# Kernel optimization log

Hardware: AMD Instinct MI355X
Metric: run time of the kernel (lower is better)

The kernel has to match this reference:

```python
import jax, jax.numpy as jnp
import numpy as np

B, S, DIM = 2, 2048, 2048
H, HKV = 16, 4
HD = DIM // H          # 128
REP = H // HKV         # 4


def _rope_cos_sin(seq_len, head_dim, theta=10000.0):
    freqs = 1.0 / (theta ** (np.arange(0, head_dim, 2, dtype=np.float32) / head_dim))
    t = np.arange(seq_len, dtype=np.float32)
    ang = np.outer(t, freqs)  # (S, HD//2)
    return jnp.asarray(np.cos(ang)), jnp.asarray(np.sin(ang))


def setup_inputs() -> dict:
    key = jax.random.key(0)
    ks = jax.random.split(key, 5)
    cos, sin = _rope_cos_sin(S, HD)
    s = 1.0 / np.sqrt(DIM)
    return {
        "x": jax.random.normal(ks[0], (B, S, DIM), jnp.float32),
        "cos": cos,
        "sin": sin,
        "wq": jax.random.normal(ks[1], (DIM, H * HD), jnp.float32) * s,
        "wk": jax.random.normal(ks[2], (DIM, HKV * HD), jnp.float32) * s,
        "wv": jax.random.normal(ks[3], (DIM, HKV * HD), jnp.float32) * s,
        "wo": jax.random.normal(ks[4], (H * HD, DIM), jnp.float32) * s,
    }


def _apply_rope(t, cos, sin):
    # t: (B, S, h, HD); interleaved pairs as in torch view_as_complex
    th = t.reshape(*t.shape[:-1], HD // 2, 2)
    t0, t1 = th[..., 0], th[..., 1]
    c = cos[None, :, None, :]
    sn = sin[None, :, None, :]
    o0 = t0 * c - t1 * sn
    o1 = t0 * sn + t1 * c
    return jnp.stack([o0, o1], axis=-1).reshape(t.shape)


def reference(x, cos, sin, wq, wk, wv, wo):
    b, s, _ = x.shape
    q = (x @ wq).reshape(b, s, H, HD)
    k = (x @ wk).reshape(b, s, HKV, HD)
    v = (x @ wv).reshape(b, s, HKV, HD)
    q = _apply_rope(q, cos, sin)
    k = _apply_rope(k, cos, sin)
    # GQA without materializing repeated KV: group query heads
    qg = q.reshape(b, s, HKV, REP, HD)  # (b, q, g, r, d)
    scale = 1.0 / np.sqrt(HD)
    scores = jnp.einsum('bqgrd,bkgd->bgrqk', qg, k) * scale  # (b,g,r,S,S)
    causal = jnp.tril(jnp.ones((s, s), dtype=bool))
    scores = jnp.where(causal, scores, -jnp.inf)
    attn = jax.nn.softmax(scores.astype(jnp.float32), axis=-1).astype(x.dtype)
    out = jnp.einsum('bgrqk,bkgd->bqgrd', attn, v)  # (b,S,g,r,d)
    out = out.reshape(b, s, H * HD)
    return out @ wo
```

## Files before the change

### kernel.cpp

```cpp
#include <hip/hip_runtime.h>
#include <cstdint>
#include <cmath>

#define B_ 2
#define S_ 2048
#define DIM_ 2048
#define H_ 16
#define HKV_ 4
#define HD_ 128
#define MQ_ (B_*S_)
#define NKV_ (HKV_*HD_)
#define NQKV_ 3072
#define KOFF_ 2048
#define VOFF_ 2560

typedef unsigned short u16;
typedef unsigned int u32;
typedef __bf16 bf16_t;
typedef bf16_t bf16x8 __attribute__((ext_vector_type(8)));
typedef bf16_t bf16x2 __attribute__((ext_vector_type(2)));
typedef u16 u16x8 __attribute__((ext_vector_type(8)));
typedef u16 u16x4 __attribute__((ext_vector_type(4)));
typedef float f32x4 __attribute__((ext_vector_type(4)));
typedef float f32x16 __attribute__((ext_vector_type(16)));
typedef u32 u32x4 __attribute__((ext_vector_type(4)));

__device__ __forceinline__ u16 f2bf(float f) {
  union { float f; uint32_t u; } v; v.f = f;
  return (u16)((v.u + 0x7FFFu + ((v.u >> 16) & 1u)) >> 16);
}

__device__ __forceinline__ u32 pkbf(float a, float b) {
  bf16x2 v; v[0] = (bf16_t)a; v[1] = (bf16_t)b;
  return __builtin_bit_cast(u32, v);
}

__device__ __forceinline__ float bf2f(u16 u) {
  union { u32 u; float f; } v; v.u = ((u32)u) << 16;
  return v.f;
}


__global__ void cvt_x_kernel(const float* __restrict__ in, u16* __restrict__ out, int n4) {
  int i = blockIdx.x * blockDim.x + threadIdx.x;
  if (i >= n4) return;
  float4 v = reinterpret_cast<const float4*>(in)[i];
  u16x4 o;
  o[0] = f2bf(v.x); o[1] = f2bf(v.y); o[2] = f2bf(v.z); o[3] = f2bf(v.w);
  reinterpret_cast<u16x4*>(out)[i] = o;
}

__global__ void wtT_all_kernel(const float* __restrict__ wq, const float* __restrict__ wk,
                               const float* __restrict__ wv, const float* __restrict__ wo,
                               u16* __restrict__ wqkvT, u16* __restrict__ woT) {
  __shared__ u16 tile[64][66];
  const int z = blockIdx.x;
  const float* src; u16* dst; int N, n0;
  if (z < 32)      { src = wq; dst = wqkvT;                          N = 2048; n0 = z * 64; }
  else if (z < 40) { src = wk; dst = wqkvT + (size_t)KOFF_ * DIM_;   N = 512;  n0 = (z - 32) * 64; }
  else if (z < 48) { src = wv; dst = wqkvT + (size_t)VOFF_ * DIM_;   N = 512;  n0 = (z - 40) * 64; }
  else             { src = wo; dst = woT;                            N = 2048; n0 = (z - 48) * 64; }
  const int k0 = blockIdx.y * 64;
  const int tx = threadIdx.x & 63, ty = threadIdx.x >> 6;
#pragma unroll
  for (int i = 0; i < 16; i++) {
    int kr = ty + i * 4;
    tile[tx][kr] = f2bf(src[(size_t)(k0 + kr) * N + n0 + tx]);
  }
  __syncthreads();
#pragma unroll
  for (int i = 0; i < 16; i++) {
    int nr = ty + i * 4;
    dst[(size_t)(n0 + nr) * DIM_ + k0 + tx] = tile[nr][tx];
  }
}

__global__ void rope_bf_kernel(u16* __restrict__ buf, const float* __restrict__ cosp,
                               const float* __restrict__ sinp, int npairs) {
  int i = blockIdx.x * blockDim.x + threadIdx.x;
  if (i >= npairs) return;
  int j = i & 63;
  int head = (i >> 6) % 20;
  int token = i / (20 * 64);
  int s = token % S_;
  u16* p = buf + (size_t)token * NQKV_ + head * HD_ + j * 2;
  u32 v = *reinterpret_cast<u32*>(p);
  float t0 = bf2f((u16)(v & 0xFFFF));
  float t1 = bf2f((u16)(v >> 16));
  float c = cosp[s * 64 + j], sn = sinp[s * 64 + j];
  u16 lo = f2bf(t0 * c - t1 * sn);
  u16 hi = f2bf(t0 * sn + t1 * c);
  *reinterpret_cast<u32*>(p) = (u32)lo | ((u32)hi << 16);
}

__global__ void vtT_kernel(const u16* __restrict__ qkv, u16* __restrict__ vt) {
  __shared__ u16 tile[64][66];
  const int s0 = blockIdx.x * 64, d0 = blockIdx.y * 64;
  const int bg = blockIdx.z, b = bg >> 2, g = bg & 3;
  const int tx = threadIdx.x & 63, ty = threadIdx.x >> 6;
#pragma unroll
  for (int i = 0; i < 16; i++) {
    int sr = ty + i * 4;
    tile[tx][sr] = qkv[(size_t)(b * S_ + s0 + sr) * NQKV_ + VOFF_ + g * HD_ + d0 + tx];
  }
  __syncthreads();
#pragma unroll
  for (int i = 0; i < 16; i++) {
    int dr = ty + i * 4;
    vt[((size_t)bg * HD_ + d0 + dr) * S_ + s0 + tx] = tile[dr][tx];
  }
}

template <int BN, typename OutT>
__launch_bounds__(512, 1)
__global__ void gemm256(const u16* __restrict__ A, const u16* __restrict__ Bt,
                        OutT* __restrict__ C, int M, int N, int K) {
  constexpr int NWN = BN / 64;
  constexpr int NWM = 8 / NWN;
  constexpr int RW  = 256 / NWM;
  constexpr int RH  = RW / 2;
  constexpr int MFR = RH / 16;
  constexpr int BHB = BN * 64;
  constexpr int BST = BHB / 8192;

  __shared__ u16 As[2][16384];
  __shared__ u16 Bs[2][BN * 64];
  const int tid = threadIdx.x;
  const int lane = tid & 63, wid = tid >> 6;
  const int lr = lane & 15, lg = lane >> 4;
  const int wm = (wid / NWN) * RW;
  const int wn = (wid % NWN) * 64;
  const int m0 = blockIdx.y * 256, n0 = blockIdx.x * BN;
  const u16* Atile = A + (size_t)m0 * K;
  const u16* Btile = Bt + (size_t)n0 * K;
  const int NT = K >> 6;
  const int NIT = NT >> 1;

  f32x4 acc[2 * MFR][4] = {};
  bf16x8 afr[MFR][2];
  bf16x8 bfr[2][2][2];

  auto stgA = [&](u16* lbase, int t, int h) {
#pragma unroll
    for (int j = 0; j < 2; j++) {
      int L = (tid + j * 512) * 16;
      int r = L >> 7;
      int slot = (L >> 4) & 7;
      int c = (slot ^ (r & 7)) << 4;
      const char* src = (const char*)(Atile + (size_t)(h * 128 + r) * K + t * 64) + c;
      __builtin_amdgcn_global_load_lds(
          (const __attribute__((address_space(1))) unsigned int*)src,
          (__attribute__((address_space(3))) unsigned int*)((char*)lbase + h * 16384 + L),
          16, 0, 0);
    }
  };
  auto stgB = [&](u16* lbase, int t, int h) {
#pragma unroll
    for (int j = 0; j < BST; j++) {
      int L = (tid + j * 512) * 16;
      int r = L >> 7;
      int slot = (L >> 4) & 7;
      int c = (slot ^ (r & 7)) << 4;
      const char* src = (const char*)(Btile + (size_t)(h * (BN / 2) + r) * K + t * 64) + c;
      __builtin_amdgcn_global_load_lds(
          (const __attribute__((address_space(1))) unsigned int*)src,
          (__attribute__((address_space(3))) unsigned int*)((char*)lbase + h * BHB + L),
          16, 0, 0);
    }
  };
  auto lds8 = [&](const u16* lbase, int r, int cb) -> bf16x8 {
    int slot = (cb >> 4) & 7;
    int L = r * 128 + ((slot ^ (r & 7)) << 4) + (cb & 15);
    return *reinterpret_cast<const bf16x8*>((const char*)lbase + L);
  };
  auto readA = [&](int buf, int mh) {
#pragma unroll
    for (int im = 0; im < MFR; im++)
#pragma unroll
      for (int k = 0; k < 2; k++)
        afr[im][k] = lds8(As[buf], wm + mh * RH + im * 16 + lr, k * 64 + lg * 16);
  };
  auto readB = [&](int buf, int nh) {
#pragma unroll
    for (int jn = 0; jn < 2; jn++)
#pragma unroll
      for (int k = 0; k < 2; k++)
        bfr[nh][jn][k] = lds8(Bs[buf], wn + nh * 32 + jn * 16 + lr, k * 64 + lg * 16);
  };
  auto quad = [&](int mh, int nh) {
    __builtin_amdgcn_s_setprio(1);
#pragma unroll
    for (int im = 0; im < MFR; im++)
#pragma unroll
      for (int jn = 0; jn < 2; jn++)
#pragma unroll
      for (int k = 0; k < 2; k++)
        acc[mh * MFR + im][nh * 2 + jn] = __builtin_amdgcn_mfma_f32_16x16x32_bf16(
            afr[im][k], bfr[nh][jn][k], acc[mh * MFR + im][nh * 2 + jn], 0, 0, 0);
    __builtin_amdgcn_s_setprio(0);
  };
  auto bar = [&]() {
    asm volatile("" ::: "memory");
    __builtin_amdgcn_s_barrier();
    asm volatile("" ::: "memory");
  };

  stgA(As[0], 0, 0); stgA(As[0], 0, 1);
  stgB(Bs[0], 0, 0); stgB(Bs[0], 0, 1);
  stgA(As[1], 1, 0);
  asm volatile("s_waitcnt vmcnt(2)" ::: "memory");
  __builtin_amdgcn_s_barrier();

  for (int it = 0; it < NIT; ++it) {
    const int ta = 2 * it, tb = ta + 1;
    const bool sA = (ta + 2 < NT);
    const bool sB = (tb + 2 < NT);

    readA(0, 0); readB(0, 0);
    stgA(As[1], tb, 1);
    bar(); quad(0, 0); bar();
    readB(0, 1);
    stgB(Bs[1], tb, 0);
    bar(); quad(0, 1); bar();
    readA(0, 1);
    stgB(Bs[1], tb, 1);
    bar(); quad(1, 1); bar();
    if (sA) stgA(As[0], ta + 2, 0);
    bar(); quad(1, 0);
    if (sA) asm volatile("s_waitcnt vmcnt(2)" ::: "memory");
    else    asm volatile("s_waitcnt vmcnt(0)" ::: "memory");
    bar();

    readA(1, 0); readB(1, 0);
    if (sA) stgA(As[0], ta + 2, 1);
    bar(); quad(0, 0); bar();
    readB(1, 1);
    if (sA) stgB(Bs[0], ta + 2, 0);
    bar(); quad(0, 1); bar();
    readA(1, 1);
    if (sA) stgB(Bs[0], ta + 2, 1);
    bar(); quad(1, 1); bar();
    if (sB) stgA(As[1], tb + 2, 0);
    bar(); quad(1, 0);
    if (sA) {
      if (sB) asm volatile("s_waitcnt vmcnt(2)" ::: "memory");
      else    asm volatile("s_waitcnt vmcnt(0)" ::: "memory");
    }
    bar();
  }

#pragma unroll
  for (int i = 0; i < 2 * MFR; i++)
#pragma unroll
    for (int j = 0; j < 4; j++)
#pragma unroll
      for (int rr = 0; rr < 4; rr++) {
        int row = m0 + wm + (i / MFR) * RH + (i % MFR) * 16 + lg * 4 + rr;
        int col = n0 + wn + (j >> 1) * 32 + (j & 1) * 16 + lr;
        if constexpr (__is_same(OutT, float))
          C[(size_t)row * N + col] = acc[i][j][rr];
        else
          C[(size_t)row * N + col] = f2bf(acc[i][j][rr]);
      }
}

__launch_bounds__(256, 2)
__global__ void attn_kernel(const u16* __restrict__ Qc, const u16* __restrict__ Kc,
                            const u16* __restrict__ Vt, u16* __restrict__ Ab) {
  __shared__ u16 Ks[2][64 * 128];
  __shared__ u16 Vs[2][128 * 64];

  const int bk = blockIdx.x;
  const int i = bk >> 3, gb = bk & 7;
  const int g = gb & 3, b = gb >> 2;
  const int qt = (i < 32) ? (63 - i) : (i - 32);
  const int w = threadIdx.x >> 6, lane = threadIdx.x & 63;
  const int l31 = lane & 31, hi = lane >> 5;
  const int h = g * 4 + w;
  const int qbase = qt * 32;
  const int qi = qbase + l31;
  const float k1 = 0.08838834764831845f * 1.4426950408889634f;

  bf16x8 qf[8];
  const u16* qptr = Qc + (size_t)(b * S_ + qi) * NQKV_ + h * HD_ + hi * 8;
#pragma unroll
  for (int dk = 0; dk < 8; dk++)
    qf[dk] = *reinterpret_cast<const bf16x8*>(qptr + dk * 16);

  f32x16 oacc[4] = {};
  float m = -INFINITY, li = 0.f;

  const char* kgb = (const char*)(Kc + (size_t)b * S_ * NQKV_ + g * HD_);
  const char* vgb = (const char*)(Vt + ((size_t)(b * HKV_ + g) * HD_) * (size_t)S_);
  const int nc = (qt >> 1) + 1;

  auto stage = [&](int buf, int kc) {
#pragma unroll
    for (int j = 0; j < 4; j++) {
      int L = (w * 4 + j) * 1024 + lane * 16;
      int key = L >> 8;
      int slot = (L >> 4) & 15;
      const char* src = kgb + (size_t)(kc + key) * (NQKV_ * 2) + ((slot ^ (key & 15)) << 4);
      __builtin_amdgcn_global_load_lds(
          (const __attribute__((address_space(1))) unsigned int*)src,
          (__attribute__((address_space(3))) unsigned int*)((char*)&Ks[buf][0] + (w * 4 + j) * 1024),
          16, 0, 0);
    }
#pragma unroll
    for (int j = 0; j < 4; j++) {
      int L = (w * 4 + j) * 1024 + lane * 16;
      int d = L >> 7;
      int slot = (L >> 4) & 7;
      const char* src = vgb + ((size_t)d * S_ + kc) * 2 + ((slot ^ (d & 7)) << 4);
      __builtin_amdgcn_global_load_lds(
          (const __attribute__((address_space(1))) unsigned int*)src,
          (__attribute__((address_space(3))) unsigned int*)((char*)&Vs[buf][0] + (w * 4 + j) * 1024),
          16, 0, 0);
    }
  };

  stage(0, 0);
  if (nc > 1) stage(1, 64);

  for (int c = 0; c < nc; ++c) {
    if (c + 1 < nc) asm volatile("s_waitcnt vmcnt(8)" ::: "memory");
    else            asm volatile("s_waitcnt vmcnt(0)" ::: "memory");
    __builtin_amdgcn_s_barrier();

    const char* kb_l = (const char*)&Ks[c & 1][0];
    const char* vb_l = (const char*)&Vs[c & 1][0];
    const int kc = c * 64;

    f32x16 sa0 = {}, sa1 = {};
#pragma unroll
    for (int dk = 0; dk < 8; dk++) {
      bf16x8 kf0 = *reinterpret_cast<const bf16x8*>(kb_l + l31 * 256 + (((dk * 2 + hi) ^ (l31 & 15)) << 4));
      sa0 = __builtin_amdgcn_mfma_f32_32x32x16_bf16(kf0, qf[dk], sa0, 0, 0, 0);
    }
#pragma unroll
    for (int dk = 0; dk < 8; dk++) {
      int key1 = 32 + l31;
      bf16x8 kf1 = *reinterpret_cast<const bf16x8*>(kb_l + key1 * 256 + (((dk * 2 + hi) ^ (key1 & 15)) << 4));
      sa1 = __builtin_amdgcn_mfma_f32_32x32x16_bf16(kf1, qf[dk], sa1, 0, 0, 0);
    }

    float t0[16], t1[16];
    const bool edge = (kc + 63 > qbase);
#pragma unroll
    for (int r = 0; r < 16; r++) {
      int kl = (r & 3) + 8 * (r >> 2) + 4 * hi;
      float v0 = sa0[r] * k1;
      float v1 = sa1[r] * k1;
      if (edge) {
        v0 = (kc + kl <= qi) ? v0 : -INFINITY;
        v1 = (kc + 32 + kl <= qi) ? v1 : -INFINITY;
      }
      t0[r] = v0; t1[r] = v1;
    }

    float mx[8];
#pragma unroll
    for (int r = 0; r < 8; r++)
      mx[r] = fmaxf(fmaxf(t0[r], t0[r + 8]), fmaxf(t1[r], t1[r + 8]));
    mx[0] = fmaxf(mx[0], mx[4]); mx[1] = fmaxf(mx[1], mx[5]);
    mx[2] = fmaxf(mx[2], mx[6]); mx[3] = fmaxf(mx[3], mx[7]);
    mx[0] = fmaxf(fmaxf(mx[0], mx[1]), fmaxf(mx[2], mx[3]));
    float tm = fmaxf(mx[0], __shfl_xor(mx[0], 32));

    if (!__all(tm <= m + 8.f)) {
      float mnew = fmaxf(m, tm);
      float corr = __builtin_amdgcn_exp2f(m - mnew);
      li *= corr;
#pragma unroll
      for (int r = 0; r < 16; r++) {
        float cc = __shfl(corr, (r & 3) + 8 * (r >> 2) + 4 * hi);
#pragma unroll
        for (int df = 0; df < 4; df++) oacc[df][r] *= cc;
      }
      m = mnew;
    }

    u32 own0[8], own1[8], oth0[8], oth1[8];
    float ps = 0.f;
#pragma unroll
    for (int s = 0; s < 8; s++) {
      float a0 = __builtin_amdgcn_exp2f(t0[2 * s] - m);
      float b0 = __builtin_amdgcn_exp2f(t0[2 * s + 1] - m);
      float a1 = __builtin_amdgcn_exp2f(t1[2 * s] - m);
      float b1 = __builtin_amdgcn_exp2f(t1[2 * s + 1] - m);
      ps += (a0 + b0) + (a1 + b1);
      own0[s] = pkbf(a0, b0);
      own1[s] = pkbf(a1, b1);
    }
    ps += __shfl_xor(ps, 32);
    li += ps;
#pragma unroll
    for (int s = 0; s < 8; s++) {
      oth0[s] = (u32)__shfl_xor((int)own0[s], 32);
      oth1[s] = (u32)__shfl_xor((int)own1[s], 32);
    }

#pragma unroll
    for (int ks = 0; ks < 4; ks++) {
      const u32* ow = (ks < 2) ? own0 : own1;
      const u32* ot = (ks < 2) ? oth0 : oth1;
      const int bo = 4 * (ks & 1);
      u32x4 pw;
      pw[0] = hi ? ot[bo + 2] : ow[bo];
      pw[1] = hi ? ot[bo + 3] : ow[bo + 1];
      pw[2] = hi ? ow[bo + 2] : ot[bo];
      pw[3] = hi ? ow[bo + 3] : ot[bo + 1];
      bf16x8 pf = __builtin_bit_cast(bf16x8, pw);
#pragma unroll
      for (int df = 0; df < 4; df++) {
        int d = df * 32 + l31;
        bf16x8 vf = *reinterpret_cast<const bf16x8*>(vb_l + d * 128 + (((ks * 2 + hi) ^ (d & 7)) << 4));
        oacc[df] = __builtin_amdgcn_mfma_f32_32x32x16_bf16(pf, vf, oacc[df], 0, 0, 0);
      }
    }

    __builtin_amdgcn_s_barrier();
    if (c + 2 < nc) stage(c & 1, kc + 128);
  }

#pragma unroll
  for (int r = 0; r < 16; r++) {
    int qrow = (r & 3) + 8 * (r >> 2) + 4 * hi;
    float lsum = __shfl(li, qrow);
    float inv = 1.f / lsum;
    u16* orow = Ab + ((size_t)((b * S_ + qbase + qrow) * H_ + h)) * HD_ + l31;
#pragma unroll
    for (int df = 0; df < 4; df++)
      orow[df * 32] = f2bf(oacc[df][r] * inv);
  }
}

extern "C" void kernel_launch(void* const* d_in, const int* in_sizes, int n_in,
                              void* d_out, int out_size, void* d_ws, size_t ws_size,
                              hipStream_t stream) {
  const float* x    = (const float*)d_in[0];
  const float* cosp = (const float*)d_in[1];
  const float* sinp = (const float*)d_in[2];
  const float* wq   = (const float*)d_in[3];
  const float* wk   = (const float*)d_in[4];
  const float* wv   = (const float*)d_in[5];
  const float* wo   = (const float*)d_in[6];
  float* out = (float*)d_out;

  char* ws = (char*)d_ws;
  size_t off = 0;
  auto alloc = [&](size_t bytes) -> void* {
    void* p = ws + off;
    off += (bytes + 255) & ~(size_t)255;
    return p;
  };
  u16* xb     = (u16*)alloc((size_t)MQ_ * DIM_ * 2);
  u16* wqkvT  = (u16*)alloc((size_t)NQKV_ * DIM_ * 2);
  u16* woT    = (u16*)alloc((size_t)DIM_ * DIM_ * 2);
  u16* Cq     = (u16*)alloc((size_t)MQ_ * NQKV_ * 2);
  u16* Vt     = (u16*)alloc((size_t)MQ_ * NKV_ * 2);
  u16* Ab     = (u16*)alloc((size_t)MQ_ * DIM_ * 2);

  const int TB = 256;
  cvt_x_kernel<<<(MQ_ * DIM_ / 4 + TB - 1) / TB, TB, 0, stream>>>(x, xb, MQ_ * DIM_ / 4);
  wtT_all_kernel<<<dim3(80, 32), TB, 0, stream>>>(wq, wk, wv, wo, wqkvT, woT);

  gemm256<256, u16><<<dim3(NQKV_ / 256, MQ_ / 256), 512, 0, stream>>>(xb, wqkvT, Cq, MQ_, NQKV_, DIM_);

  rope_bf_kernel<<<(MQ_ * 20 * 64 + TB - 1) / TB, TB, 0, stream>>>(Cq, cosp, sinp, MQ_ * 20 * 64);
  vtT_kernel<<<dim3(S_ / 64, HD_ / 64, B_ * HKV_), TB, 0, stream>>>(Cq, Vt);

  attn_kernel<<<dim3(64 * 8), TB, 0, stream>>>(Cq, Cq + KOFF_, Vt, Ab);

  gemm256<128, float><<<dim3(DIM_ / 128, MQ_ / 256), 512, 0, stream>>>(Ab, woT, out, MQ_, DIM_, DIM_);
}
```

Before: 210.0 us.

## Split long causal attention query tiles across two blocks with combine pass

Query tiles in the upper half of the sequence now have their KV chunks divided between two workgroups. Each workgroup writes a normalized partial output plus running max and sum, and a new combine kernel merges the two partials into the attention output. This evens out per-block work and raises the grid from 512 to 768 blocks to improve load balance on the GPU. In exchange it adds a kernel launch, extra global traffic for the bf16 partials, and an extra bf16 rounding step.

Result: no change. 211.7 us (+0.8%).

```diff
diff --git a/kernel.cpp b/kernel.cpp
--- a/kernel.cpp
+++ b/kernel.cpp
@@ -266,14 +266,19 @@
 
 __launch_bounds__(256, 2)
 __global__ void attn_kernel(const u16* __restrict__ Qc, const u16* __restrict__ Kc,
-                            const u16* __restrict__ Vt, u16* __restrict__ Ab) {
+                            const u16* __restrict__ Vt, u16* __restrict__ Ab,
+                            u16* __restrict__ P0, u16* __restrict__ P1,
+                            float2* __restrict__ ML0, float2* __restrict__ ML1) {
   __shared__ u16 Ks[2][64 * 128];
   __shared__ u16 Vs[2][128 * 64];
 
   const int bk = blockIdx.x;
-  const int i = bk >> 3, gb = bk & 7;
+  const bool split = (bk < 512);
+  int qt, half = 0;
+  if (split) { int u = bk >> 3; qt = 63 - (u >> 1); half = u & 1; }
+  else       { int u = (bk - 512) >> 3; qt = 31 - u; }
+  const int gb = bk & 7;
   const int g = gb & 3, b = gb >> 2;
-  const int qt = (i < 32) ? (63 - i) : (i - 32);
   const int w = threadIdx.x >> 6, lane = threadIdx.x & 63;
   const int l31 = lane & 31, hi = lane >> 5;
   const int h = g * 4 + w;
@@ -281,6 +286,11 @@
   const int qi = qbase + l31;
   const float k1 = 0.08838834764831845f * 1.4426950408889634f;
 
+  const int ncT = (qt >> 1) + 1;
+  const int h1 = (ncT + 1) >> 1;
+  const int c0   = split ? (half ? h1 : 0) : 0;
+  const int cend = split ? (half ? ncT : h1) : ncT;
+
   bf16x8 qf[8];
   const u16* qptr = Qc + (size_t)(b * S_ + qi) * NQKV_ + h * HD_ + hi * 8;
 #pragma unroll
@@ -292,7 +302,6 @@
 
   const char* kgb = (const char*)(Kc + (size_t)b * S_ * NQKV_ + g * HD_);
   const char* vgb = (const char*)(Vt + ((size_t)(b * HKV_ + g) * HD_) * (size_t)S_);
-  const int nc = (qt >> 1) + 1;
 
   auto stage = [&](int buf, int kc) {
 #pragma unroll
@@ -319,16 +328,17 @@
     }
   };
 
-  stage(0, 0);
-  if (nc > 1) stage(1, 64);
-
-  for (int c = 0; c < nc; ++c) {
-    if (c + 1 < nc) asm volatile("s_waitcnt vmcnt(8)" ::: "memory");
-    else            asm volatile("s_waitcnt vmcnt(0)" ::: "memory");
+  stage(0, c0 * 64);
+  if (cend - c0 > 1) stage(1, (c0 + 1) * 64);
+
+  for (int c = c0; c < cend; ++c) {
+    const int cc = c - c0;
+    if (c + 1 < cend) asm volatile("s_waitcnt vmcnt(8)" ::: "memory");
+    else              asm volatile("s_waitcnt vmcnt(0)" ::: "memory");
     __builtin_amdgcn_s_barrier();
 
-    const char* kb_l = (const char*)&Ks[c & 1][0];
-    const char* vb_l = (const char*)&Vs[c & 1][0];
+    const char* kb_l = (const char*)&Ks[cc & 1][0];
+    const char* vb_l = (const char*)&Vs[cc & 1][0];
     const int kc = c * 64;
 
     f32x16 sa0 = {}, sa1 = {};
@@ -373,9 +383,9 @@
       li *= corr;
 #pragma unroll
       for (int r = 0; r < 16; r++) {
-        float cc = __shfl(corr, (r & 3) + 8 * (r >> 2) + 4 * hi);
-#pragma unroll
-        for (int df = 0; df < 4; df++) oacc[df][r] *= cc;
+        float cc2 = __shfl(corr, (r & 3) + 8 * (r >> 2) + 4 * hi);
+#pragma unroll
+        for (int df = 0; df < 4; df++) oacc[df][r] *= cc2;
       }
       m = mnew;
     }
@@ -420,19 +430,66 @@
     }
 
     __builtin_amdgcn_s_barrier();
-    if (c + 2 < nc) stage(c & 1, kc + 128);
-  }
-
-#pragma unroll
-  for (int r = 0; r < 16; r++) {
-    int qrow = (r & 3) + 8 * (r >> 2) + 4 * hi;
-    float lsum = __shfl(li, qrow);
-    float inv = 1.f / lsum;
-    u16* orow = Ab + ((size_t)((b * S_ + qbase + qrow) * H_ + h)) * HD_ + l31;
-#pragma unroll
-    for (int df = 0; df < 4; df++)
-      orow[df * 32] = f2bf(oacc[df][r] * inv);
-  }
+    if (c + 2 < cend) stage(cc & 1, kc + 128);
+  }
+
+  if (split) {
+    u16* pb = half ? P1 : P0;
+    float2* ml = half ? ML1 : ML0;
+    const int srel = qbase - S_ / 2;
+#pragma unroll
+    for (int r = 0; r < 16; r++) {
+      int qrow = (r & 3) + 8 * (r >> 2) + 4 * hi;
+      float lsum = __shfl(li, qrow);
+      float inv = 1.f / lsum;
+      u16* orow = pb + ((size_t)((b * (S_ / 2) + srel + qrow) * H_) + h) * HD_ + l31;
+#pragma unroll
+      for (int df = 0; df < 4; df++)
+        orow[df * 32] = f2bf(oacc[df][r] * inv);
+    }
+    if (lane < 32) {
+      float2 v; v.x = m; v.y = li;
+      ml[((size_t)(b * H_ + h)) * (S_ / 2) + srel + lane] = v;
+    }
+  } else {
+#pragma unroll
+    for (int r = 0; r < 16; r++) {
+      int qrow = (r & 3) + 8 * (r >> 2) + 4 * hi;
+      float lsum = __shfl(li, qrow);
+      float inv = 1.f / lsum;
+      u16* orow = Ab + ((size_t)((b * S_ + qbase + qrow) * H_ + h)) * HD_ + l31;
+#pragma unroll
+      for (int df = 0; df < 4; df++)
+        orow[df * 32] = f2bf(oacc[df][r] * inv);
+    }
+  }
+}
+
+__global__ void attn_combine_kernel(const u16* __restrict__ P0, const u16* __restrict__ P1,
+                                    const float2* __restrict__ ML0, const float2* __restrict__ ML1,
+                                    u16* __restrict__ Ab) {
+  int t = blockIdx.x * blockDim.x + threadIdx.x;
+  if (t >= B_ * (S_ / 2) * H_ * (HD_ / 8)) return;
+  int d8 = t & 15;
+  int h  = (t >> 4) & 15;
+  int sr = (t >> 8) & 1023;
+  int b  = t >> 18;
+  size_t poff = ((size_t)((b * (S_ / 2) + sr) * H_) + h) * HD_ + d8 * 8;
+  size_t mli  = ((size_t)(b * H_ + h)) * (S_ / 2) + sr;
+  float2 a0 = ML0[mli], a1 = ML1[mli];
+  float M = fmaxf(a0.x, a1.x);
+  float w0 = a0.y * __builtin_amdgcn_exp2f(a0.x - M);
+  float w1 = a1.y * __builtin_amdgcn_exp2f(a1.x - M);
+  float inv = 1.f / (w0 + w1);
+  w0 *= inv; w1 *= inv;
+  u16x8 v0 = *reinterpret_cast<const u16x8*>(P0 + poff);
+  u16x8 v1 = *reinterpret_cast<const u16x8*>(P1 + poff);
+  u16x8 o;
+#pragma unroll
+  for (int j = 0; j < 8; j++)
+    o[j] = f2bf(bf2f(v0[j]) * w0 + bf2f(v1[j]) * w1);
+  size_t aoff = ((size_t)((b * S_ + S_ / 2 + sr) * H_) + h) * HD_ + d8 * 8;
+  *reinterpret_cast<u16x8*>(Ab + aoff) = o;
 }
 
 extern "C" void kernel_launch(void* const* d_in, const int* in_sizes, int n_in,
@@ -460,6 +517,10 @@
   u16* Cq     = (u16*)alloc((size_t)MQ_ * NQKV_ * 2);
   u16* Vt     = (u16*)alloc((size_t)MQ_ * NKV_ * 2);
   u16* Ab     = (u16*)alloc((size_t)MQ_ * DIM_ * 2);
+  u16* P0     = (u16*)alloc((size_t)B_ * (S_ / 2) * DIM_ * 2);
+  u16* P1     = (u16*)alloc((size_t)B_ * (S_ / 2) * DIM_ * 2);
+  float2* ML0 = (float2*)alloc((size_t)B_ * H_ * (S_ / 2) * 8);
+  float2* ML1 = (float2*)alloc((size_t)B_ * H_ * (S_ / 2) * 8);
 
   const int TB = 256;
   cvt_x_kernel<<<(MQ_ * DIM_ / 4 + TB - 1) / TB, TB, 0, stream>>>(x, xb, MQ_ * DIM_ / 4);
@@ -470,7 +531,8 @@
   rope_bf_kernel<<<(MQ_ * 20 * 64 + TB - 1) / TB, TB, 0, stream>>>(Cq, cosp, sinp, MQ_ * 20 * 64);
   vtT_kernel<<<dim3(S_ / 64, HD_ / 64, B_ * HKV_), TB, 0, stream>>>(Cq, Vt);
 
-  attn_kernel<<<dim3(64 * 8), TB, 0, stream>>>(Cq, Cq + KOFF_, Vt, Ab);
+  attn_kernel<<<dim3(768), TB, 0, stream>>>(Cq, Cq + KOFF_, Vt, Ab, P0, P1, ML0, ML1);
+  attn_combine_kernel<<<(B_ * (S_ / 2) * H_ * (HD_ / 8) + TB - 1) / TB, TB, 0, stream>>>(P0, P1, ML0, ML1, Ab);
 
   gemm256<128, float><<<dim3(DIM_ / 128, MQ_ / 256), 512, 0, stream>>>(Ab, woT, out, MQ_, DIM_, DIM_);
 }
```
